# Kernel tuning notes

Measured on AMD Instinct MI355X. Metric: run time of the kernel, lower is better.

## Reference

```python
import jax, jax.numpy as jnp
import numpy as np


def setup_inputs() -> dict:
    key = jax.random.key(0)
    k1, k2, k3, k4 = jax.random.split(key, 4)
    B, S, D = 16, 1024, 300      # batch, set_size, word_vector_dim
    K = 64                        # hidden_set_size == compressed_dim (element_dim)
    O = 256                       # set_representation_dim (output_dim)
    Xs = jax.random.normal(k1, (B, S, D), dtype=jnp.float32)
    # Linear(word_vector_dim -> hidden_set_size)
    W = jax.random.normal(k2, (K, D), dtype=jnp.float32) * (1.0 / np.sqrt(D))
    b = jax.random.normal(k3, (K,), dtype=jnp.float32) * 0.01
    # hidden_sets: (output_dim, hidden_set_size, element_dim) with xavier-normal scale
    xav = np.sqrt(2.0 / (K + K))
    hidden_sets = jax.random.normal(k4, (O, K, K), dtype=jnp.float32) * xav
    return {"Xs": Xs, "W": W, "b": b, "hidden_sets": hidden_sets}


def reference(Xs, W, b, hidden_sets):
    # compress: [B,S,D] @ [D,K] + b -> [B,S,K]
    Xc = jnp.einsum('bsd,kd->bsk', Xs, W) + b
    # bipartite_match: tensordot over element_dim -> [B,S,O,N] (N = hidden_set_size)
    G = jax.nn.relu(jnp.einsum('bsk,onk->bson', Xc, hidden_sets))
    # set_size (1024) > hidden_set_size (64): max over hidden-set axis, sum over set axis
    value = jnp.sum(jnp.max(G, axis=-1), axis=1)  # [B,O]
    return value
```

## Files before the change

kernel.cpp:

```cpp
#include <hip/hip_runtime.h>
#include <hip/hip_bf16.h>

#define B_  16
#define S_  1024
#define D_  300
#define DP  320
#define K_  64
#define O_  256
#define M_  (B_*S_)

typedef __attribute__((ext_vector_type(8)))  short s8b;
typedef __attribute__((ext_vector_type(4)))  float f32x4;
typedef __attribute__((ext_vector_type(16))) float f32x16;

#define MFMA16(a,b,c) __builtin_amdgcn_mfma_f32_16x16x32_bf16((a),(b),(c),0,0,0)
#define MFMA32(a,b,c) __builtin_amdgcn_mfma_f32_32x32x16_bf16((a),(b),(c),0,0,0)

__device__ __forceinline__ unsigned short bf16_bits(float f) {
    return __builtin_bit_cast(unsigned short, __float2bfloat16(f));
}

#define H_BLK  512
#define W_BLK  10
__global__ __launch_bounds__(256) void k_convert(
        const float* __restrict__ W, const float* __restrict__ H,
        __hip_bfloat16* __restrict__ Wb, __hip_bfloat16* __restrict__ Hb) {
    int bx = blockIdx.x, t = threadIdx.x;
    if (bx < H_BLK) {
        int g = (bx * 256 + t) * 8;
        float4 f0 = *(const float4*)(H + g);
        float4 f1 = *(const float4*)(H + g + 4);
        union { unsigned short us[8]; uint4 q; } pk;
        pk.us[0]=bf16_bits(f0.x); pk.us[1]=bf16_bits(f0.y);
        pk.us[2]=bf16_bits(f0.z); pk.us[3]=bf16_bits(f0.w);
        pk.us[4]=bf16_bits(f1.x); pk.us[5]=bf16_bits(f1.y);
        pk.us[6]=bf16_bits(f1.z); pk.us[7]=bf16_bits(f1.w);
        *(uint4*)(Hb + g) = pk.q;
        return;
    }
    int g = (bx - H_BLK) * 256 + t;
    int r = g / 40, c = (g - r * 40) * 8;
    const float* src = W + (size_t)r * D_;
    float v[8];
    if (c + 8 <= D_) {
        float4 f0 = *(const float4*)(src + c);
        float4 f1 = *(const float4*)(src + c + 4);
        v[0]=f0.x; v[1]=f0.y; v[2]=f0.z; v[3]=f0.w;
        v[4]=f1.x; v[5]=f1.y; v[6]=f1.z; v[7]=f1.w;
    } else {
#pragma unroll
        for (int j = 0; j < 8; ++j) v[j] = (c + j < D_) ? src[c + j] : 0.0f;
    }
    union { unsigned short us[8]; uint4 q; } pk;
#pragma unroll
    for (int j = 0; j < 8; ++j) pk.us[j] = bf16_bits(v[j]);
    *(uint4*)(Wb + (size_t)r * DP + c) = pk.q;
}

__global__ __launch_bounds__(256) void k_compress(
        const float* __restrict__ Xs,
        const __hip_bfloat16* __restrict__ Wb,
        const float* __restrict__ bias,
        __hip_bfloat16* __restrict__ Xc) {
    int tid  = threadIdx.x;
    int w    = tid >> 6, lane = tid & 63;
    int q    = lane >> 4, r = lane & 15;
    int row0 = blockIdx.x * 16;
    int col0 = w * 16;

    f32x4 acc0 = {0.f,0.f,0.f,0.f}, acc1 = {0.f,0.f,0.f,0.f};
    const float*          arow = Xs + (size_t)(row0 + r) * D_;
    const __hip_bfloat16* brow = Wb + (size_t)(col0 + r) * DP;
    const float4 z4 = {0.f,0.f,0.f,0.f};

#pragma unroll
    for (int ks = 0; ks < 10; ++ks) {
        int k0 = ks * 32 + q * 8;
        float4 f0 = (k0     < D_) ? *(const float4*)(arow + k0)     : z4;
        float4 f1 = (k0 + 4 < D_) ? *(const float4*)(arow + k0 + 4) : z4;
        union { unsigned short us[8]; s8b v; } pk;
        pk.us[0]=bf16_bits(f0.x); pk.us[1]=bf16_bits(f0.y);
        pk.us[2]=bf16_bits(f0.z); pk.us[3]=bf16_bits(f0.w);
        pk.us[4]=bf16_bits(f1.x); pk.us[5]=bf16_bits(f1.y);
        pk.us[6]=bf16_bits(f1.z); pk.us[7]=bf16_bits(f1.w);
        s8b b = __builtin_bit_cast(s8b, *(const uint4*)(brow + k0));
        if (ks & 1) acc1 = MFMA16(pk.v, b, acc1);
        else        acc0 = MFMA16(pk.v, b, acc0);
    }
#pragma unroll
    for (int i = 0; i < 4; ++i) {
        int orow = row0 + q * 4 + i;
        int c    = col0 + r;
        Xc[(size_t)orow * K_ + c] =
            __float2bfloat16(acc0[i] + acc1[i] + bias[c]);
    }
}

__global__ __launch_bounds__(256, 4) void k_fused(
        const __hip_bfloat16* __restrict__ Xc,
        const __hip_bfloat16* __restrict__ Hb,
        float* __restrict__ out) {
    __shared__ __hip_bfloat16 lx[128 * 64];
    int tid   = threadIdx.x;
    int w     = tid >> 6, lane = tid & 63;
    int half  = lane >> 5, l31 = lane & 31;
    int bx    = blockIdx.x;
    int batch = bx >> 6;
    int oq    = bx & 63;
    int o     = oq * 4 + w;

    s8b af[2][4];
#pragma unroll
    for (int nt = 0; nt < 2; ++nt) {
        const __hip_bfloat16* hrow =
            Hb + (size_t)(o * 64 + nt * 32 + l31) * 64 + half * 8;
#pragma unroll
        for (int ks = 0; ks < 4; ++ks)
            af[nt][ks] = __builtin_bit_cast(s8b, *(const uint4*)(hrow + ks * 16));
    }

    int sr = tid >> 3, sc = tid & 7;
    const __hip_bfloat16* xbase = Xc + (size_t)batch * S_ * K_;

#pragma unroll
    for (int i = 0; i < 4; ++i) {
        int r = sr + i * 32;
        uint4 v = *(const uint4*)(xbase + (size_t)r * 64 + sc * 8);
        *(uint4*)(&lx[r * 64 + (sc ^ (r & 7)) * 8]) = v;
    }

    float total = 0.0f;
    for (int it = 0; it < 8; ++it) {
        __syncthreads();
        uint4 npf[4];
        if (it < 7) {
            const __hip_bfloat16* nsrc = xbase + (size_t)(it + 1) * 128 * 64;
#pragma unroll
            for (int i = 0; i < 4; ++i)
                npf[i] = *(const uint4*)(nsrc + (size_t)(sr + i * 32) * 64 + sc * 8);
        }
#pragma unroll
        for (int t = 0; t < 4; ++t) {
            int rr = t * 32 + l31;
            int sw = rr & 7;
            s8b bf[4];
#pragma unroll
            for (int ks = 0; ks < 4; ++ks)
                bf[ks] = __builtin_bit_cast(s8b,
                    *(const uint4*)(&lx[rr * 64 + ((2 * ks + half) ^ sw) * 8]));

            f32x16 a0 = {0.f,0.f,0.f,0.f,0.f,0.f,0.f,0.f,
                         0.f,0.f,0.f,0.f,0.f,0.f,0.f,0.f};
            f32x16 a1 = a0;
#pragma unroll
            for (int ks = 0; ks < 4; ++ks) {
                a0 = MFMA32(af[0][ks], bf[ks], a0);
                a1 = MFMA32(af[1][ks], bf[ks], a1);
            }
            float m0 = fmaxf(fmaxf(a0[0], a0[1]),  fmaxf(a0[2], a0[3]));
            float m1 = fmaxf(fmaxf(a0[4], a0[5]),  fmaxf(a0[6], a0[7]));
            float m2 = fmaxf(fmaxf(a0[8], a0[9]),  fmaxf(a0[10], a0[11]));
            float m3 = fmaxf(fmaxf(a0[12], a0[13]),fmaxf(a0[14], a0[15]));
            float n0 = fmaxf(fmaxf(a1[0], a1[1]),  fmaxf(a1[2], a1[3]));
            float n1 = fmaxf(fmaxf(a1[4], a1[5]),  fmaxf(a1[6], a1[7]));
            float n2 = fmaxf(fmaxf(a1[8], a1[9]),  fmaxf(a1[10], a1[11]));
            float n3 = fmaxf(fmaxf(a1[12], a1[13]),fmaxf(a1[14], a1[15]));
            float v  = fmaxf(fmaxf(fmaxf(m0, m1), fmaxf(m2, m3)),
                             fmaxf(fmaxf(n0, n1), fmaxf(n2, n3)));
            v = fmaxf(v, __shfl_xor(v, 32));
            v = fmaxf(v, 0.0f);
            total += v;
        }
        __syncthreads();
        if (it < 7) {
#pragma unroll
            for (int i = 0; i < 4; ++i) {
                int r = sr + i * 32;
                *(uint4*)(&lx[r * 64 + (sc ^ (r & 7)) * 8]) = npf[i];
            }
        }
    }
    total += __shfl_xor(total, 1);
    total += __shfl_xor(total, 2);
    total += __shfl_xor(total, 4);
    total += __shfl_xor(total, 8);
    total += __shfl_xor(total, 16);
    if (lane == 0) out[batch * O_ + o] = total;
}

extern "C" void kernel_launch(void* const* d_in, const int* in_sizes, int n_in,
                              void* d_out, int out_size, void* d_ws, size_t ws_size,
                              hipStream_t stream) {
    const float* Xs   = (const float*)d_in[0];
    const float* W    = (const float*)d_in[1];
    const float* bias = (const float*)d_in[2];
    const float* H    = (const float*)d_in[3];
    float* out = (float*)d_out;

    char* ws = (char*)d_ws;
    __hip_bfloat16* Wb = (__hip_bfloat16*)(ws);
    __hip_bfloat16* Hb = (__hip_bfloat16*)(ws + 40960);
    __hip_bfloat16* Xc = (__hip_bfloat16*)(ws + 2138112);

    k_convert <<<H_BLK + W_BLK, 256, 0, stream>>>(W, H, Wb, Hb);
    k_compress<<<M_ / 16, 256, 0, stream>>>(Xs, Wb, bias, Xc);
    k_fused   <<<B_ * (O_ / 4), 256, 0, stream>>>(Xc, Hb, out);
}
```

Before: 123.9 us.

## Split set axis across two blocks with atomic accumulation, drop LDS staging

The fused kernel now splits each batch's 1024-element set into two halves handled by separate blocks, doubling the grid, and accumulates partial sums into the output with atomicAdd. An extra block in the convert kernel zeroes the output first. The LDS staging and double-buffered prefetch with barriers are removed, so each wave loads its B fragments directly from global memory (relying on L2/L1 reuse), and the cross-lane shuffles are batched four at a time. It trades LDS reuse and swizzled loads for more parallelism and no synchronisation, at the risk of redundant global traffic and atomic contention.

```diff
diff --git a/kernel.cpp b/kernel.cpp
--- a/kernel.cpp
+++ b/kernel.cpp
@@ -24,7 +24,8 @@
 #define W_BLK  10
 __global__ __launch_bounds__(256) void k_convert(
         const float* __restrict__ W, const float* __restrict__ H,
-        __hip_bfloat16* __restrict__ Wb, __hip_bfloat16* __restrict__ Hb) {
+        __hip_bfloat16* __restrict__ Wb, __hip_bfloat16* __restrict__ Hb,
+        float* __restrict__ out) {
     int bx = blockIdx.x, t = threadIdx.x;
     if (bx < H_BLK) {
         int g = (bx * 256 + t) * 8;
@@ -36,6 +37,13 @@
         pk.us[4]=bf16_bits(f1.x); pk.us[5]=bf16_bits(f1.y);
         pk.us[6]=bf16_bits(f1.z); pk.us[7]=bf16_bits(f1.w);
         *(uint4*)(Hb + g) = pk.q;
+        return;
+    }
+    if (bx == H_BLK + W_BLK) {
+        float4 z = {0.f,0.f,0.f,0.f};
+        float4* o4 = (float4*)out;
+#pragma unroll
+        for (int i = 0; i < 4; ++i) o4[t * 4 + i] = z;
         return;
     }
     int g = (bx - H_BLK) * 256 + t;
@@ -96,17 +104,17 @@
     }
 }
 
-__global__ __launch_bounds__(256, 4) void k_fused(
+__global__ __launch_bounds__(256) void k_fused(
         const __hip_bfloat16* __restrict__ Xc,
         const __hip_bfloat16* __restrict__ Hb,
         float* __restrict__ out) {
-    __shared__ __hip_bfloat16 lx[128 * 64];
     int tid   = threadIdx.x;
     int w     = tid >> 6, lane = tid & 63;
     int half  = lane >> 5, l31 = lane & 31;
     int bx    = blockIdx.x;
-    int batch = bx >> 6;
-    int oq    = bx & 63;
+    int batch = bx >> 7;
+    int oq    = (bx >> 1) & 63;
+    int sh    = bx & 1;
     int o     = oq * 4 + w;
 
     s8b af[2][4];
@@ -119,35 +127,21 @@
             af[nt][ks] = __builtin_bit_cast(s8b, *(const uint4*)(hrow + ks * 16));
     }
 
-    int sr = tid >> 3, sc = tid & 7;
-    const __hip_bfloat16* xbase = Xc + (size_t)batch * S_ * K_;
-
-#pragma unroll
-    for (int i = 0; i < 4; ++i) {
-        int r = sr + i * 32;
-        uint4 v = *(const uint4*)(xbase + (size_t)r * 64 + sc * 8);
-        *(uint4*)(&lx[r * 64 + (sc ^ (r & 7)) * 8]) = v;
-    }
+    const __hip_bfloat16* xbase =
+        Xc + ((size_t)batch * S_ + (size_t)sh * 512) * K_;
 
     float total = 0.0f;
-    for (int it = 0; it < 8; ++it) {
-        __syncthreads();
-        uint4 npf[4];
-        if (it < 7) {
-            const __hip_bfloat16* nsrc = xbase + (size_t)(it + 1) * 128 * 64;
+    for (int tt = 0; tt < 4; ++tt) {
+        float vt[4];
 #pragma unroll
-            for (int i = 0; i < 4; ++i)
-                npf[i] = *(const uint4*)(nsrc + (size_t)(sr + i * 32) * 64 + sc * 8);
-        }
-#pragma unroll
-        for (int t = 0; t < 4; ++t) {
+        for (int j = 0; j < 4; ++j) {
+            int t  = tt * 4 + j;
             int rr = t * 32 + l31;
-            int sw = rr & 7;
+            const __hip_bfloat16* xrow = xbase + (size_t)rr * K_ + half * 8;
             s8b bf[4];
 #pragma unroll
             for (int ks = 0; ks < 4; ++ks)
-                bf[ks] = __builtin_bit_cast(s8b,
-                    *(const uint4*)(&lx[rr * 64 + ((2 * ks + half) ^ sw) * 8]));
+                bf[ks] = __builtin_bit_cast(s8b, *(const uint4*)(xrow + ks * 16));
 
             f32x16 a0 = {0.f,0.f,0.f,0.f,0.f,0.f,0.f,0.f,
                          0.f,0.f,0.f,0.f,0.f,0.f,0.f,0.f};
@@ -165,27 +159,22 @@
             float n1 = fmaxf(fmaxf(a1[4], a1[5]),  fmaxf(a1[6], a1[7]));
             float n2 = fmaxf(fmaxf(a1[8], a1[9]),  fmaxf(a1[10], a1[11]));
             float n3 = fmaxf(fmaxf(a1[12], a1[13]),fmaxf(a1[14], a1[15]));
-            float v  = fmaxf(fmaxf(fmaxf(m0, m1), fmaxf(m2, m3)),
-                             fmaxf(fmaxf(n0, n1), fmaxf(n2, n3)));
-            v = fmaxf(v, __shfl_xor(v, 32));
-            v = fmaxf(v, 0.0f);
-            total += v;
+            vt[j] = fmaxf(fmaxf(fmaxf(m0, m1), fmaxf(m2, m3)),
+                          fmaxf(fmaxf(n0, n1), fmaxf(n2, n3)));
         }
-        __syncthreads();
-        if (it < 7) {
 #pragma unroll
-            for (int i = 0; i < 4; ++i) {
-                int r = sr + i * 32;
-                *(uint4*)(&lx[r * 64 + (sc ^ (r & 7)) * 8]) = npf[i];
-            }
-        }
+        for (int j = 0; j < 4; ++j)
+            vt[j] = fmaxf(vt[j], __shfl_xor(vt[j], 32));
+#pragma unroll
+        for (int j = 0; j < 4; ++j)
+            total += fmaxf(vt[j], 0.0f);
     }
     total += __shfl_xor(total, 1);
     total += __shfl_xor(total, 2);
     total += __shfl_xor(total, 4);
     total += __shfl_xor(total, 8);
     total += __shfl_xor(total, 16);
-    if (lane == 0) out[batch * O_ + o] = total;
+    if (lane == 0) atomicAdd(out + batch * O_ + o, total);
 }
 
 extern "C" void kernel_launch(void* const* d_in, const int* in_sizes, int n_in,
@@ -202,7 +191,7 @@
     __hip_bfloat16* Hb = (__hip_bfloat16*)(ws + 40960);
     __hip_bfloat16* Xc = (__hip_bfloat16*)(ws + 2138112);
 
-    k_convert <<<H_BLK + W_BLK, 256, 0, stream>>>(W, H, Wb, Hb);
+    k_convert <<<H_BLK + W_BLK + 1, 256, 0, stream>>>(W, H, Wb, Hb, out);
     k_compress<<<M_ / 16, 256, 0, stream>>>(Xs, Wb, bias, Xc);
-    k_fused   <<<B_ * (O_ / 4), 256, 0, stream>>>(Xc, Hb, out);
+    k_fused   <<<B_ * (O_ / 4) * 2, 256, 0, stream>>>(Xc, Hb, out);
 }
```

Measured after the change: 146.8 us. 18.5% more time.
